# Optimization experiments

Measured on AMD Instinct MI355X. Metric: run time of the kernel, lower is better.

## Reference

```python
import jax, jax.numpy as jnp
import numpy as np

MAX_BOXES = 50
NOOBJ_SCALE = 1.0
OBJ_SCALE = 5.0
COORD_SCALE = 1.0
CLASS_SCALE = 1.0
SIL_THRESH = 0.6


def setup_inputs() -> dict:
    key = jax.random.key(0)
    k1, k2, k3, k4 = jax.random.split(key, 4)
    nB, nA, nC, nH, nW = 32, 5, 20, 64, 64
    output = jax.random.normal(k1, (nB, nA * (5 + nC), nH, nW), jnp.float32) * 0.5
    # targets: 12 valid boxes per image, rest zero (loop-break semantics)
    K = 12
    cls = jax.random.randint(k2, (nB, MAX_BOXES, 1), 0, nC).astype(jnp.float32)
    xy = jax.random.uniform(k3, (nB, MAX_BOXES, 2), minval=0.05, maxval=0.95)
    wh = jax.random.uniform(k4, (nB, MAX_BOXES, 2), minval=0.05, maxval=0.3)
    boxes = jnp.concatenate([cls, xy, wh], axis=-1)          # [nB, 50, 5]
    valid = (jnp.arange(MAX_BOXES) < K)[None, :, None].astype(jnp.float32)
    target = (boxes * valid).reshape(nB, MAX_BOXES * 5)
    anchors = jnp.array([1.3221, 1.73145, 3.19275, 4.00944, 5.05587,
                         8.09892, 9.47112, 4.84053, 11.2364, 10.0071], jnp.float32)
    return {"output": output, "target": target, "anchors": anchors}


def _iou(b1, b2):
    # center-format boxes (cx, cy, w, h) on the last axis, broadcastable
    l = jnp.maximum(b1[..., 0] - b1[..., 2] * 0.5, b2[..., 0] - b2[..., 2] * 0.5)
    r = jnp.minimum(b1[..., 0] + b1[..., 2] * 0.5, b2[..., 0] + b2[..., 2] * 0.5)
    t = jnp.maximum(b1[..., 1] - b1[..., 3] * 0.5, b2[..., 1] - b2[..., 3] * 0.5)
    b = jnp.minimum(b1[..., 1] + b1[..., 3] * 0.5, b2[..., 1] + b2[..., 3] * 0.5)
    inter = jnp.clip(r - l, 0.0) * jnp.clip(b - t, 0.0)
    union = b1[..., 2] * b1[..., 3] + b2[..., 2] * b2[..., 3] - inter
    return inter / jnp.maximum(union, 1e-10)


def reference(output, target, anchors):
    nB, _, nH, nW = output.shape
    nA = anchors.shape[0] // 2
    nC = output.shape[1] // nA - 5
    out = output.reshape(nB, nA, 5 + nC, nH, nW)

    x = jax.nn.sigmoid(out[:, :, 0])            # [nB,nA,nH,nW]
    y = jax.nn.sigmoid(out[:, :, 1])
    w = out[:, :, 2]
    h = out[:, :, 3]
    conf = jax.nn.sigmoid(out[:, :, 4])
    cls_logits = jnp.transpose(out[:, :, 5:], (0, 1, 3, 4, 2))  # [nB,nA,nH,nW,nC]

    aw = anchors[0::2]
    ah = anchors[1::2]
    grid_x = jnp.arange(nW, dtype=output.dtype)
    grid_y = jnp.arange(nH, dtype=output.dtype)[:, None]
    px = x + grid_x
    py = y + grid_y
    pw = jnp.exp(w) * aw[None, :, None, None]
    ph = jnp.exp(h) * ah[None, :, None, None]
    # build_targets consumes pred_boxes.data -> no grad through it
    pred = jax.lax.stop_gradient(jnp.stack([px, py, pw, ph], axis=-1))  # [nB,nA,nH,nW,4]

    tgt = target.reshape(nB, -1, 5)             # (cls, x, y, w, h)
    T = tgt.shape[1]
    valid = tgt[:, :, 1] > 0
    gx = tgt[:, :, 1] * nW
    gy = tgt[:, :, 2] * nH
    gw = tgt[:, :, 3] * nW
    gh = tgt[:, :, 4] * nH
    gboxes = jnp.stack([gx, gy, gw, gh], axis=-1)  # [nB,T,4]

    # conf_mask: zero out anchors whose IoU with any gt exceeds sil_thresh
    pred_flat = pred.reshape(nB, nA * nH * nW, 4)
    ious = _iou(pred_flat[:, :, None, :], gboxes[:, None, :, :])   # [nB,nAnchors,T]
    max_iou = jnp.max(jnp.where(valid[:, None, :], ious, 0.0), axis=-1)
    conf_base = jnp.where(max_iou.reshape(nB, nA, nH, nW) > SIL_THRESH, 0.0, NOOBJ_SCALE)

    # best anchor per gt: IoU of (0,0,gw,gh) vs (0,0,aw,ah)
    inter_a = jnp.minimum(gw[..., None], aw) * jnp.minimum(gh[..., None], ah)
    iou_a = inter_a / jnp.maximum(gw[..., None] * gh[..., None] + aw * ah - inter_a, 1e-10)
    best_n = jnp.argmax(iou_a, axis=-1)          # [nB,T]

    gi = jnp.clip(jnp.floor(gx), 0, nW - 1).astype(jnp.int32)
    gj = jnp.clip(jnp.floor(gy), 0, nH - 1).astype(jnp.int32)
    bidx = jnp.arange(nB)[:, None]
    N = nB * nA * nH * nW
    flat = ((bidx * nA + best_n) * nH + gj) * nW + gi
    flat = jnp.where(valid, flat, N).reshape(-1)   # invalid gts go to dummy slot N

    def scat(base, vals):
        padded = jnp.concatenate([base.reshape(-1), jnp.zeros((1,), base.dtype)])
        return padded.at[flat].set(vals.reshape(-1))[:N].reshape(nB, nA, nH, nW)

    zeros4 = jnp.zeros((nB, nA, nH, nW), output.dtype)
    half4 = jnp.full((nB, nA, nH, nW), 0.5, output.dtype)
    # seen < 12800 branch: coord_mask all ones, tx=ty=0.5, tw=th=0 as base
    coord_mask = jnp.ones((nB, nA, nH, nW), output.dtype)
    tx = scat(half4, gx - gi.astype(output.dtype))
    ty = scat(half4, gy - gj.astype(output.dtype))
    tw = scat(zeros4, jnp.log(jnp.maximum(gw, 1e-10) / aw[best_n]))
    th = scat(zeros4, jnp.log(jnp.maximum(gh, 1e-10) / ah[best_n]))
    cls_mask = scat(zeros4, jnp.ones((nB, T), output.dtype))
    conf_mask = scat(conf_base, jnp.full((nB, T), OBJ_SCALE, output.dtype))

    pred_pad = jnp.concatenate([pred.reshape(N, 4), jnp.zeros((1, 4), pred.dtype)])
    psel = pred_pad[flat]                         # [nB*T,4]
    iou_gt = _iou(gboxes.reshape(-1, 4), psel)
    tconf = scat(zeros4, iou_gt)
    tcls = scat(zeros4, tgt[:, :, 0])

    tx, ty, tw, th, tconf = map(jax.lax.stop_gradient, (tx, ty, tw, th, tconf))

    cm = coord_mask
    loss_x = COORD_SCALE * 0.5 * jnp.sum((x * cm - tx * cm) ** 2)
    loss_y = COORD_SCALE * 0.5 * jnp.sum((y * cm - ty * cm) ** 2)
    loss_w = COORD_SCALE * 0.5 * jnp.sum((w * cm - tw * cm) ** 2)
    loss_h = COORD_SCALE * 0.5 * jnp.sum((h * cm - th * cm) ** 2)
    sq = jnp.sqrt(conf_mask)
    loss_conf = 0.5 * jnp.sum((conf * sq - tconf * sq) ** 2)
    logp = jax.nn.log_softmax(cls_logits, axis=-1)
    picked = jnp.take_along_axis(logp, tcls.astype(jnp.int32)[..., None], axis=-1)[..., 0]
    loss_cls = CLASS_SCALE * (-(picked * cls_mask).sum())
    return loss_x + loss_y + loss_w + loss_h + loss_conf + loss_cls
```

## Files before the change

kernel.cpp:

```cpp
#include <hip/hip_runtime.h>
#include <math.h>

#define NB 32
#define NA 5
#define NC 20
#define NH 64
#define NW 64
#define MAXB 50
#define CELLS_PER_BLOCK 512
#define BLOCKS_PER_BATCH 40
#define NBLK 1280
#define OBJ_SCALE 5.0f
#define SILC 0.375f
#define POISON_I ((int)0xAAAAAAAA)

#define WS_CTR_IDX NBLK

__device__ __forceinline__ float fsig(float v) {
    return __builtin_amdgcn_rcpf(1.0f + __expf(-v));
}

__device__ __forceinline__ float iou_full(float x1, float y1, float w1, float h1,
                                          float x2, float y2, float w2, float h2) {
    float l = fmaxf(x1 - 0.5f * w1, x2 - 0.5f * w2);
    float r = fminf(x1 + 0.5f * w1, x2 + 0.5f * w2);
    float t = fmaxf(y1 - 0.5f * h1, y2 - 0.5f * h2);
    float b = fminf(y1 + 0.5f * h1, y2 + 0.5f * h2);
    float inter = fmaxf(r - l, 0.0f) * fmaxf(b - t, 0.0f);
    float uni = w1 * h1 + w2 * h2 - inter;
    return inter / fmaxf(uni, 1e-10f);
}

__global__ __launch_bounds__(256) void region_all(
        const float* __restrict__ out, const float* __restrict__ target,
        const float* __restrict__ anchors, float* __restrict__ ws,
        float* __restrict__ loss) {
    __shared__ float s_t[MAXB * 5];
    __shared__ float s_box[250];
    __shared__ int s_flat[64];
    __shared__ int s_nv;
    __shared__ int s_last;
    __shared__ float s_p[4];

    const int tid = threadIdx.x;
    const int blk = blockIdx.x;
    const int b = blk / BLOCKS_PER_BATCH;
    const int rb = blk - b * BLOCKS_PER_BATCH;

    const float* tg = target + b * MAXB * 5;
    if (tid < 250) s_t[tid] = tg[tid];
    __syncthreads();

    float v = 0.0f;

    if (tid < 64) {
        bool valid = false;
        float gx = 0, gy = 0, gw = 0, gh = 0, clsf = 0;
        if (tid < MAXB) {
            clsf = s_t[tid * 5 + 0];
            float xx = s_t[tid * 5 + 1];
            gx = xx * 64.0f;
            gy = s_t[tid * 5 + 2] * 64.0f;
            gw = s_t[tid * 5 + 3] * 64.0f;
            gh = s_t[tid * 5 + 4] * 64.0f;
            valid = xx > 0.0f;
        }
        unsigned long long mask = __ballot(valid);
        int pos = __popcll(mask & ((1ull << tid) - 1ull));
        int nv = __popcll(mask);
        if (valid) {
            s_box[pos]       = gx - 0.5f * gw;
            s_box[50 + pos]  = gx + 0.5f * gw;
            s_box[100 + pos] = gy - 0.5f * gh;
            s_box[150 + pos] = gy + 0.5f * gh;
            s_box[200 + pos] = SILC * gw * gh;
        }
        if (tid == 0) s_nv = nv;

        if (rb == 0) {
            float aw_[NA], ah_[NA];
            for (int q = 0; q < NA; ++q) { aw_[q] = anchors[2 * q]; ah_[q] = anchors[2 * q + 1]; }
            int best_n = 0, gi = 0, gj = 0, myflat = -1;
            if (valid) {
                float besti = -1.0f;
                for (int q = 0; q < NA; ++q) {
                    float inter = fminf(gw, aw_[q]) * fminf(gh, ah_[q]);
                    float iou = inter / fmaxf(gw * gh + aw_[q] * ah_[q] - inter, 1e-10f);
                    if (iou > besti) { besti = iou; best_n = q; }
                }
                gi = min(max((int)floorf(gx), 0), 63);
                gj = min(max((int)floorf(gy), 0), 63);
                myflat = (best_n << 12) | (gj << 6) | gi;
            }
            s_flat[tid] = myflat;

            bool winner = (myflat >= 0);
            if (winner) {
                for (int t2 = tid + 1; t2 < MAXB; ++t2)
                    if (s_flat[t2] == myflat) { winner = false; break; }
            }
            if (winner) {
                const float* basep = out + ((size_t)(b * 125 + best_n * 25) << 12)
                                   + (gj << 6) + gi;
                float xr = basep[0];
                float yr = basep[1 * 4096];
                float wr = basep[2 * 4096];
                float hr = basep[3 * 4096];
                float cr = basep[4 * 4096];

                float x = fsig(xr), y = fsig(yr), conf = fsig(cr);
                float aw = aw_[best_n], ah = ah_[best_n];
                float pw = __expf(wr) * aw, ph = __expf(hr) * ah;
                float px = x + (float)gi, py = y + (float)gj;
                float pl = px - 0.5f * pw, pr2 = px + 0.5f * pw;
                float pt = py - 0.5f * ph, pb2 = py + 0.5f * ph;
                float pa375 = SILC * (pw * ph);

                bool hit = false;
                for (int k = 0; k < nv; ++k) {
                    float l = fmaxf(pl, s_box[k]);
                    float r = fminf(pr2, s_box[50 + k]);
                    float t = fmaxf(pt, s_box[100 + k]);
                    float bo = fminf(pb2, s_box[150 + k]);
                    float inter = fmaxf(r - l, 0.0f) * fmaxf(bo - t, 0.0f);
                    hit = hit || (inter > pa375 + s_box[200 + k]);
                }
                float cb = hit ? 0.0f : 1.0f;

                float txv = gx - (float)gi;
                float tyv = gy - (float)gj;
                float twv = __logf(fmaxf(gw, 1e-10f) / aw);
                float thv = __logf(fmaxf(gh, 1e-10f) / ah);
                float tconf = iou_full(gx, gy, gw, gh, px, py, pw, ph);

                float dxn = x - txv, dyn = y - tyv, dwn = wr - twv, dhn = hr - thv;
                float dxo = x - 0.5f, dyo = y - 0.5f;
                float dc = conf - tconf;

                v += 0.5f * ((dxn * dxn - dxo * dxo) + (dyn * dyn - dyo * dyo)
                           + (dwn * dwn - wr * wr) + (dhn * dhn - hr * hr))
                   + 0.5f * (OBJ_SCALE * dc * dc - cb * conf * conf);

                const float* cl = basep + 5 * 4096;
                float lg[NC];
                float m = -INFINITY;
                for (int c = 0; c < NC; ++c) { lg[c] = cl[c * 4096]; m = fmaxf(m, lg[c]); }
                float s = 0.0f;
                for (int c = 0; c < NC; ++c) s += __expf(lg[c] - m);
                int ci = (int)clsf;
                v -= (lg[ci] - m - __logf(s));
            }
        }
    }
    __syncthreads();

    const int a = rb >> 3;
    const int ji0 = (rb & 7) * CELLS_PER_BLOCK;
    const float aw = anchors[2 * a], ah = anchors[2 * a + 1];
    const float* obase = out + ((size_t)(b * 125 + a * 25) << 12);
    const int nv = s_nv;

    #pragma unroll
    for (int c = 0; c < 2; ++c) {
        int cell = ji0 + tid + c * 256;
        int i = cell & 63, j = (cell >> 6) & 63;
        const float* base = obase + cell;
        float xr = base[0];
        float yr = base[1 * 4096];
        float wr = base[2 * 4096];
        float hr = base[3 * 4096];
        float cr = base[4 * 4096];

        float x = fsig(xr), y = fsig(yr), conf = fsig(cr);
        float pw = __expf(wr) * aw, ph = __expf(hr) * ah;
        float px = x + (float)i, py = y + (float)j;
        float pl = px - 0.5f * pw, pr2 = px + 0.5f * pw;
        float pt = py - 0.5f * ph, pb2 = py + 0.5f * ph;
        float pa375 = SILC * (pw * ph);

        bool hit = false;
        for (int k = 0; k < nv; ++k) {
            float l = fmaxf(pl, s_box[k]);
            float r = fminf(pr2, s_box[50 + k]);
            float t = fmaxf(pt, s_box[100 + k]);
            float bo = fminf(pb2, s_box[150 + k]);
            float inter = fmaxf(r - l, 0.0f) * fmaxf(bo - t, 0.0f);
            hit = hit || (inter > pa375 + s_box[200 + k]);
        }
        float cb = hit ? 0.0f : 1.0f;

        float dx = x - 0.5f, dy = y - 0.5f;
        v += 0.5f * (dx * dx + dy * dy + wr * wr + hr * hr)
           + 0.5f * cb * conf * conf;
    }

    for (int off = 32; off; off >>= 1) v += __shfl_down(v, off);
    if ((tid & 63) == 0) s_p[tid >> 6] = v;
    __syncthreads();
    if (tid == 0) {
        ws[blk] = s_p[0] + s_p[1] + s_p[2] + s_p[3];
        __threadfence();
        int old = atomicAdd((int*)ws + WS_CTR_IDX, 1);
        s_last = (old == POISON_I + NBLK - 1) || (old == NBLK - 1);
    }
    __syncthreads();

    if (s_last) {
        __threadfence();
        float t = 0.0f;
        for (int idx = tid; idx < NBLK; idx += 256) t += ws[idx];
        for (int off = 32; off; off >>= 1) t += __shfl_down(t, off);
        if ((tid & 63) == 0) s_p[tid >> 6] = t;
        __syncthreads();
        if (tid == 0) loss[0] = s_p[0] + s_p[1] + s_p[2] + s_p[3];
    }
}

extern "C" void kernel_launch(void* const* d_in, const int* in_sizes, int n_in,
                              void* d_out, int out_size, void* d_ws, size_t ws_size,
                              hipStream_t stream) {
    (void)in_sizes; (void)n_in; (void)ws_size; (void)out_size;
    const float* output  = (const float*)d_in[0];
    const float* target  = (const float*)d_in[1];
    const float* anchors = (const float*)d_in[2];
    float* ws = (float*)d_ws;
    float* loss = (float*)d_out;

    region_all<<<NBLK, 256, 0, stream>>>(output, target, anchors, ws, loss);
}
```

Measured before the change: 123.9 us.

## Prefetch cell loads before setup, fuse box loop, split final reduction kernel

The ten per-thread cell loads are issued at kernel entry, ahead of the target loading and the per-box setup, so global-memory latency overlaps with that setup. The two cells now share one pass over the ground-truth boxes, which halves the shared-memory box reads. The last-block atomic counter and threadfence reduction is replaced by a second single-block kernel that sums the partials. This drops the atomic and fence work but adds a kernel launch and raises register pressure.

```diff
diff --git a/kernel.cpp b/kernel.cpp
--- a/kernel.cpp
+++ b/kernel.cpp
@@ -12,9 +12,6 @@
 #define NBLK 1280
 #define OBJ_SCALE 5.0f
 #define SILC 0.375f
-#define POISON_I ((int)0xAAAAAAAA)
-
-#define WS_CTR_IDX NBLK
 
 __device__ __forceinline__ float fsig(float v) {
     return __builtin_amdgcn_rcpf(1.0f + __expf(-v));
@@ -31,21 +28,27 @@
     return inter / fmaxf(uni, 1e-10f);
 }
 
-__global__ __launch_bounds__(256) void region_all(
+__global__ __launch_bounds__(256) void region_main(
         const float* __restrict__ out, const float* __restrict__ target,
-        const float* __restrict__ anchors, float* __restrict__ ws,
-        float* __restrict__ loss) {
+        const float* __restrict__ anchors, float* __restrict__ ws) {
     __shared__ float s_t[MAXB * 5];
     __shared__ float s_box[250];
     __shared__ int s_flat[64];
     __shared__ int s_nv;
-    __shared__ int s_last;
     __shared__ float s_p[4];
 
     const int tid = threadIdx.x;
     const int blk = blockIdx.x;
     const int b = blk / BLOCKS_PER_BATCH;
     const int rb = blk - b * BLOCKS_PER_BATCH;
+
+    const int a = rb >> 3;
+    const int ji0 = (rb & 7) * CELLS_PER_BLOCK;
+    const float* obase = out + ((size_t)(b * 125 + a * 25) << 12);
+    const float* b0 = obase + ji0 + tid;
+    const float* b1 = b0 + 256;
+    float xr0 = b0[0], yr0 = b0[4096], wr0 = b0[2 * 4096], hr0 = b0[3 * 4096], cr0 = b0[4 * 4096];
+    float xr1 = b1[0], yr1 = b1[4096], wr1 = b1[2 * 4096], hr1 = b1[3 * 4096], cr1 = b1[4 * 4096];
 
     const float* tg = target + b * MAXB * 5;
     if (tid < 250) s_t[tid] = tg[tid];
@@ -154,66 +157,66 @@
     }
     __syncthreads();
 
-    const int a = rb >> 3;
-    const int ji0 = (rb & 7) * CELLS_PER_BLOCK;
     const float aw = anchors[2 * a], ah = anchors[2 * a + 1];
-    const float* obase = out + ((size_t)(b * 125 + a * 25) << 12);
     const int nv = s_nv;
 
-    #pragma unroll
-    for (int c = 0; c < 2; ++c) {
-        int cell = ji0 + tid + c * 256;
-        int i = cell & 63, j = (cell >> 6) & 63;
-        const float* base = obase + cell;
-        float xr = base[0];
-        float yr = base[1 * 4096];
-        float wr = base[2 * 4096];
-        float hr = base[3 * 4096];
-        float cr = base[4 * 4096];
-
-        float x = fsig(xr), y = fsig(yr), conf = fsig(cr);
-        float pw = __expf(wr) * aw, ph = __expf(hr) * ah;
-        float px = x + (float)i, py = y + (float)j;
-        float pl = px - 0.5f * pw, pr2 = px + 0.5f * pw;
-        float pt = py - 0.5f * ph, pb2 = py + 0.5f * ph;
-        float pa375 = SILC * (pw * ph);
-
-        bool hit = false;
-        for (int k = 0; k < nv; ++k) {
-            float l = fmaxf(pl, s_box[k]);
-            float r = fminf(pr2, s_box[50 + k]);
-            float t = fmaxf(pt, s_box[100 + k]);
-            float bo = fminf(pb2, s_box[150 + k]);
-            float inter = fmaxf(r - l, 0.0f) * fmaxf(bo - t, 0.0f);
-            hit = hit || (inter > pa375 + s_box[200 + k]);
-        }
-        float cb = hit ? 0.0f : 1.0f;
-
-        float dx = x - 0.5f, dy = y - 0.5f;
-        v += 0.5f * (dx * dx + dy * dy + wr * wr + hr * hr)
-           + 0.5f * cb * conf * conf;
+    int cell0 = ji0 + tid;
+    int i0 = cell0 & 63, j0 = (cell0 >> 6) & 63;
+    int cell1 = cell0 + 256;
+    int i1 = cell1 & 63, j1 = (cell1 >> 6) & 63;
+
+    float x0 = fsig(xr0), y0 = fsig(yr0), c0 = fsig(cr0);
+    float x1 = fsig(xr1), y1 = fsig(yr1), c1 = fsig(cr1);
+    float pw0 = __expf(wr0) * aw, ph0 = __expf(hr0) * ah;
+    float pw1 = __expf(wr1) * aw, ph1 = __expf(hr1) * ah;
+    float px0 = x0 + (float)i0, py0 = y0 + (float)j0;
+    float px1 = x1 + (float)i1, py1 = y1 + (float)j1;
+    float pl0 = px0 - 0.5f * pw0, pr0 = px0 + 0.5f * pw0;
+    float pt0 = py0 - 0.5f * ph0, pb0 = py0 + 0.5f * ph0;
+    float pl1 = px1 - 0.5f * pw1, pr1 = px1 + 0.5f * pw1;
+    float pt1 = py1 - 0.5f * ph1, pb1 = py1 + 0.5f * ph1;
+    float pa0 = SILC * (pw0 * ph0);
+    float pa1 = SILC * (pw1 * ph1);
+
+    bool hit0 = false, hit1 = false;
+    for (int k = 0; k < nv; ++k) {
+        float bl = s_box[k];
+        float br = s_box[50 + k];
+        float bt = s_box[100 + k];
+        float bb = s_box[150 + k];
+        float th = s_box[200 + k];
+        float in0 = fmaxf(fminf(pr0, br) - fmaxf(pl0, bl), 0.0f)
+                  * fmaxf(fminf(pb0, bb) - fmaxf(pt0, bt), 0.0f);
+        float in1 = fmaxf(fminf(pr1, br) - fmaxf(pl1, bl), 0.0f)
+                  * fmaxf(fminf(pb1, bb) - fmaxf(pt1, bt), 0.0f);
+        hit0 = hit0 || (in0 > pa0 + th);
+        hit1 = hit1 || (in1 > pa1 + th);
     }
+
+    float dx0 = x0 - 0.5f, dy0 = y0 - 0.5f;
+    float dx1 = x1 - 0.5f, dy1 = y1 - 0.5f;
+    v += 0.5f * (dx0 * dx0 + dy0 * dy0 + wr0 * wr0 + hr0 * hr0)
+       + 0.5f * (hit0 ? 0.0f : 1.0f) * c0 * c0
+       + 0.5f * (dx1 * dx1 + dy1 * dy1 + wr1 * wr1 + hr1 * hr1)
+       + 0.5f * (hit1 ? 0.0f : 1.0f) * c1 * c1;
 
     for (int off = 32; off; off >>= 1) v += __shfl_down(v, off);
     if ((tid & 63) == 0) s_p[tid >> 6] = v;
     __syncthreads();
-    if (tid == 0) {
+    if (tid == 0)
         ws[blk] = s_p[0] + s_p[1] + s_p[2] + s_p[3];
-        __threadfence();
-        int old = atomicAdd((int*)ws + WS_CTR_IDX, 1);
-        s_last = (old == POISON_I + NBLK - 1) || (old == NBLK - 1);
-    }
-    __syncthreads();
-
-    if (s_last) {
-        __threadfence();
-        float t = 0.0f;
-        for (int idx = tid; idx < NBLK; idx += 256) t += ws[idx];
-        for (int off = 32; off; off >>= 1) t += __shfl_down(t, off);
-        if ((tid & 63) == 0) s_p[tid >> 6] = t;
-        __syncthreads();
-        if (tid == 0) loss[0] = s_p[0] + s_p[1] + s_p[2] + s_p[3];
-    }
+}
+
+__global__ __launch_bounds__(256) void region_reduce(
+        const float* __restrict__ ws, float* __restrict__ loss) {
+    __shared__ float s_p[4];
+    const int tid = threadIdx.x;
+    float v = 0.0f;
+    for (int idx = tid; idx < NBLK; idx += 256) v += ws[idx];
+    for (int off = 32; off; off >>= 1) v += __shfl_down(v, off);
+    if ((tid & 63) == 0) s_p[tid >> 6] = v;
+    __syncthreads();
+    if (tid == 0) loss[0] = s_p[0] + s_p[1] + s_p[2] + s_p[3];
 }
 
 extern "C" void kernel_launch(void* const* d_in, const int* in_sizes, int n_in,
@@ -226,5 +229,6 @@
     float* ws = (float*)d_ws;
     float* loss = (float*)d_out;
 
-    region_all<<<NBLK, 256, 0, stream>>>(output, target, anchors, ws, loss);
-}
+    region_main<<<NBLK, 256, 0, stream>>>(output, target, anchors, ws);
+    region_reduce<<<1, 256, 0, stream>>>(ws, loss);
+}
```

New measurement: 100.6 us. 18.8% less time.
